# Kernel optimization log

Hardware: AMD Instinct MI355X
Metric: run time of the kernel (lower is better)

Reference implementation:

```python
import jax, jax.numpy as jnp
import numpy as np

B, S, D, H = 2, 2048, 1024, 16
DH = D // H
LN_EPS = 1e-12


def setup_inputs() -> dict:
    key = jax.random.key(0)
    ks = jax.random.split(key, 12)
    sc = 1.0 / np.sqrt(D)
    return {
        "hidden_states": jax.random.normal(ks[0], (B, S, D), jnp.float32),
        "attention_mask": jnp.zeros((B, 1, 1, S), jnp.float32),
        "Wq": jax.random.normal(ks[1], (D, D), jnp.float32) * sc,
        "bq": jnp.zeros((D,), jnp.float32),
        "Wk": jax.random.normal(ks[2], (D, D), jnp.float32) * sc,
        "bk": jnp.zeros((D,), jnp.float32),
        "Wv": jax.random.normal(ks[3], (D, D), jnp.float32) * sc,
        "bv": jnp.zeros((D,), jnp.float32),
        "Wo": jax.random.normal(ks[4], (D, D), jnp.float32) * sc,
        "bo": jnp.zeros((D,), jnp.float32),
        "ln_w": jnp.ones((D,), jnp.float32),
        "ln_b": jnp.zeros((D,), jnp.float32),
    }


def _split_heads(x):
    # [B,S,D] -> [B,H,S,DH]
    return x.reshape(B, S, H, DH).transpose(0, 2, 1, 3)


def reference(hidden_states, attention_mask, Wq, bq, Wk, bk, Wv, bv, Wo, bo, ln_w, ln_b):
    q = _split_heads(hidden_states @ Wq + bq)
    k = _split_heads(hidden_states @ Wk + bk)
    v = _split_heads(hidden_states @ Wv + bv)
    scores = jnp.einsum("bhqd,bhkd->bhqk", q, k) / np.sqrt(DH)
    scores = scores + attention_mask
    probs = jax.nn.softmax(scores, axis=-1)  # dropout prob=0 -> identity
    ctx = jnp.einsum("bhqk,bhkd->bhqd", probs, v)
    ctx = ctx.transpose(0, 2, 1, 3).reshape(B, S, D)
    # output dense + residual + LayerNorm (biased variance, per original)
    h = ctx @ Wo + bo + hidden_states
    u = h.mean(-1, keepdims=True)
    s = ((h - u) ** 2).mean(-1, keepdims=True)
    out = ln_w * ((h - u) / jnp.sqrt(s + LN_EPS)) + ln_b
    return out, probs
```

## Files before the change

### kernel.cpp

```cpp
#include <hip/hip_runtime.h>
#include <stdint.h>


typedef __attribute__((ext_vector_type(8))) short short8;
typedef __attribute__((ext_vector_type(4))) float f32x4;

__device__ __forceinline__ unsigned short f2b(float f) {
  union { float f; unsigned u; } v; v.f = f;
  unsigned u = v.u;
  return (unsigned short)((u + 0x7fffu + ((u >> 16) & 1u)) >> 16);
}

__global__ void k_cast_hs(const float* __restrict__ x, unsigned short* __restrict__ y, int n4) {
  int i = blockIdx.x * blockDim.x + threadIdx.x;
  if (i < n4) {
    float4 v = ((const float4*)x)[i];
    ushort4 o;
    o.x = f2b(v.x); o.y = f2b(v.y); o.z = f2b(v.z); o.w = f2b(v.w);
    ((ushort4*)y)[i] = o;
  }
}

__global__ void k_transpose_cast(const float* __restrict__ Wq, const float* __restrict__ Wk,
                                 const float* __restrict__ Wv, const float* __restrict__ Wo,
                                 unsigned short* __restrict__ Tq, unsigned short* __restrict__ Tk,
                                 unsigned short* __restrict__ Tv, unsigned short* __restrict__ To) {
  __shared__ float tile[32][33];
  const float* W; unsigned short* T;
  switch (blockIdx.z) {
    case 0: W = Wq; T = Tq; break;
    case 1: W = Wk; T = Tk; break;
    case 2: W = Wv; T = Tv; break;
    default: W = Wo; T = To; break;
  }
  int n0 = blockIdx.x * 32, k0 = blockIdx.y * 32;
  int tx = threadIdx.x, ty = threadIdx.y;
#pragma unroll
  for (int j = 0; j < 4; ++j)
    tile[ty + j * 8][tx] = W[(size_t)(k0 + ty + j * 8) * 1024 + n0 + tx];
  __syncthreads();
#pragma unroll
  for (int j = 0; j < 4; ++j)
    T[(size_t)(n0 + ty + j * 8) * 1024 + k0 + tx] = f2b(tile[tx][ty + j * 8]);
}

template <int MODE>
__global__ __launch_bounds__(256) void k_gemm(const unsigned short* __restrict__ A,
                                              const unsigned short* __restrict__ Bt, int Kd,
                                              const float* __restrict__ bias,
                                              const float* __restrict__ resid,
                                              void* __restrict__ outp) {
  __shared__ __align__(16) unsigned short Asm[128 * 32];
  __shared__ __align__(16) unsigned short Bsm[128 * 32];
  const int t = threadIdx.x, w = t >> 6, l = t & 63;
  const int m0 = blockIdx.y * 128, n0 = blockIdx.x * 128;
  const int wr = w >> 1, wc = w & 1;
  const int lr = l & 15, lg = l >> 4;

  f32x4 acc[4][4];
#pragma unroll
  for (int mi = 0; mi < 4; ++mi)
#pragma unroll
    for (int ni = 0; ni < 4; ++ni) acc[mi][ni] = (f32x4){0.f, 0.f, 0.f, 0.f};

  const int kcol = (l & 3) * 8;
  for (int kt = 0; kt < Kd / 32; ++kt) {
    const int k0 = kt * 32;
#pragma unroll
    for (int i = 0; i < 2; ++i) {
      int ra = (i * 4 + w) * 16 + (l >> 2);
      const unsigned short* ga = A + (size_t)(m0 + ra) * Kd + k0 + kcol;
      __builtin_amdgcn_global_load_lds((const __attribute__((address_space(1))) void*)ga,
                                       (__attribute__((address_space(3))) void*)((char*)Asm + (i * 4 + w) * 1024),
                                       16, 0, 0);
      const unsigned short* gb = Bt + (size_t)(n0 + ra) * Kd + k0 + kcol;
      __builtin_amdgcn_global_load_lds((const __attribute__((address_space(1))) void*)gb,
                                       (__attribute__((address_space(3))) void*)((char*)Bsm + (i * 4 + w) * 1024),
                                       16, 0, 0);
    }
    __syncthreads();
    short8 af[4], bfv[4];
#pragma unroll
    for (int mi = 0; mi < 4; ++mi)
      af[mi] = *(const short8*)&Asm[(wr * 64 + mi * 16 + lr) * 32 + lg * 8];
#pragma unroll
    for (int ni = 0; ni < 4; ++ni)
      bfv[ni] = *(const short8*)&Bsm[(wc * 64 + ni * 16 + lr) * 32 + lg * 8];
#pragma unroll
    for (int mi = 0; mi < 4; ++mi)
#pragma unroll
      for (int ni = 0; ni < 4; ++ni)
        acc[mi][ni] = __builtin_amdgcn_mfma_f32_16x16x32_bf16(af[mi], bfv[ni], acc[mi][ni], 0, 0, 0);
    __syncthreads();
  }

#pragma unroll
  for (int mi = 0; mi < 4; ++mi) {
#pragma unroll
    for (int ni = 0; ni < 4; ++ni) {
#pragma unroll
      for (int r = 0; r < 4; ++r) {
        int row = m0 + wr * 64 + mi * 16 + lg * 4 + r;
        int col = n0 + wc * 64 + ni * 16 + lr;
        float v = acc[mi][ni][r];
        if constexpr (MODE == 0) {
          v += bias[col];
          int b = row >> 11, s = row & 2047, h = col >> 6, dh = col & 63;
          ((unsigned short*)outp)[((size_t)((b * 16 + h) * 2048 + s)) * 64 + dh] = f2b(v);
        } else if constexpr (MODE == 1) {
          v += bias[row];
          int h = row >> 6, dh = row & 63, b = col >> 11, s = col & 2047;
          ((unsigned short*)outp)[((size_t)((b * 16 + h) * 64 + dh)) * 2048 + s] = f2b(v);
        } else {
          v += bias[col] + resid[(size_t)row * 1024 + col];
          ((float*)outp)[(size_t)row * 1024 + col] = v;
        }
      }
    }
  }
}

__global__ __launch_bounds__(256) void k_attn(const unsigned short* __restrict__ Q,
                                              const unsigned short* __restrict__ K,
                                              const unsigned short* __restrict__ VT,
                                              const float* __restrict__ mask,
                                              float* __restrict__ probs,
                                              unsigned short* __restrict__ ctx) {
  __shared__ float smax[4][16];
  __shared__ float ssum[4][16];
  __shared__ __align__(16) unsigned short pbuf[4][16][264];
  __shared__ float redbuf[4][16][64];

  const int t = threadIdx.x, w = t >> 6, l = t & 63;
  const int qb = blockIdx.x, h = blockIdx.y, b = blockIdx.z;
  const int q0 = qb * 16;
  const int lr = l & 15, lg = l >> 4;
  const size_t head = ((size_t)(b * 16 + h)) * 2048 * 64;
  const unsigned short* Qh = Q + head + (size_t)q0 * 64;
  const unsigned short* Kh = K + head;
  const unsigned short* VTh = VT + head;

  short8 aq0 = *(const short8*)(Qh + lr * 64 + lg * 8);
  short8 aq1 = *(const short8*)(Qh + lr * 64 + 32 + lg * 8);

  f32x4 sc[32];
  const float scale = 0.125f;
#pragma unroll
  for (int ni = 0; ni < 32; ++ni) {
    int col = w * 512 + ni * 16 + lr;
    short8 bk0 = *(const short8*)(Kh + (size_t)col * 64 + lg * 8);
    short8 bk1 = *(const short8*)(Kh + (size_t)col * 64 + 32 + lg * 8);
    f32x4 c = (f32x4){0.f, 0.f, 0.f, 0.f};
    c = __builtin_amdgcn_mfma_f32_16x16x32_bf16(aq0, bk0, c, 0, 0, 0);
    c = __builtin_amdgcn_mfma_f32_16x16x32_bf16(aq1, bk1, c, 0, 0, 0);
    float mval = mask[b * 2048 + col];
#pragma unroll
    for (int r = 0; r < 4; ++r) sc[ni][r] = c[r] * scale + mval;
  }

  float vmax[4] = {-1e30f, -1e30f, -1e30f, -1e30f};
#pragma unroll
  for (int ni = 0; ni < 32; ++ni)
#pragma unroll
    for (int r = 0; r < 4; ++r) vmax[r] = fmaxf(vmax[r], sc[ni][r]);
#pragma unroll
  for (int off = 8; off >= 1; off >>= 1)
#pragma unroll
    for (int r = 0; r < 4; ++r) vmax[r] = fmaxf(vmax[r], __shfl_xor(vmax[r], off));
  if (lr == 0) {
#pragma unroll
    for (int r = 0; r < 4; ++r) smax[w][lg * 4 + r] = vmax[r];
  }
  __syncthreads();
  float m[4];
#pragma unroll
  for (int r = 0; r < 4; ++r) {
    int row = lg * 4 + r;
    m[r] = fmaxf(fmaxf(smax[0][row], smax[1][row]), fmaxf(smax[2][row], smax[3][row]));
  }
  float vsum[4] = {0.f, 0.f, 0.f, 0.f};
#pragma unroll
  for (int ni = 0; ni < 32; ++ni)
#pragma unroll
    for (int r = 0; r < 4; ++r) {
      float p = __expf(sc[ni][r] - m[r]);
      sc[ni][r] = p;
      vsum[r] += p;
    }
#pragma unroll
  for (int off = 8; off >= 1; off >>= 1)
#pragma unroll
    for (int r = 0; r < 4; ++r) vsum[r] += __shfl_xor(vsum[r], off);
  if (lr == 0) {
#pragma unroll
    for (int r = 0; r < 4; ++r) ssum[w][lg * 4 + r] = vsum[r];
  }
  __syncthreads();
  float rinv[4];
#pragma unroll
  for (int r = 0; r < 4; ++r) {
    int row = lg * 4 + r;
    rinv[r] = 1.f / (ssum[0][row] + ssum[1][row] + ssum[2][row] + ssum[3][row]);
  }

#pragma unroll
  for (int ni = 0; ni < 32; ++ni) {
#pragma unroll
    for (int r = 0; r < 4; ++r) {
      sc[ni][r] *= rinv[r];
      int row = q0 + lg * 4 + r;
      int col = w * 512 + ni * 16 + lr;
      probs[((size_t)((b * 16 + h) * 2048 + row)) * 2048 + col] = sc[ni][r];
    }
  }

  f32x4 cacc[4];
#pragma unroll
  for (int n = 0; n < 4; ++n) cacc[n] = (f32x4){0.f, 0.f, 0.f, 0.f};

#pragma unroll
  for (int chunk = 0; chunk < 2; ++chunk) {
#pragma unroll
    for (int ni2 = 0; ni2 < 16; ++ni2) {
      int ni = chunk * 16 + ni2;
#pragma unroll
      for (int r = 0; r < 4; ++r)
        pbuf[w][lg * 4 + r][ni2 * 16 + lr] = f2b(sc[ni][r]);
    }
    __syncthreads();
#pragma unroll
    for (int kc = 0; kc < 8; ++kc) {
      short8 pa = *(const short8*)&pbuf[w][lr][kc * 32 + lg * 8];
      size_t kg = (size_t)w * 512 + chunk * 256 + kc * 32;
#pragma unroll
      for (int n = 0; n < 4; ++n) {
        short8 bv = *(const short8*)(VTh + (size_t)(n * 16 + lr) * 2048 + kg + lg * 8);
        cacc[n] = __builtin_amdgcn_mfma_f32_16x16x32_bf16(pa, bv, cacc[n], 0, 0, 0);
      }
    }
    __syncthreads();
  }

#pragma unroll
  for (int n = 0; n < 4; ++n)
#pragma unroll
    for (int r = 0; r < 4; ++r)
      redbuf[w][lg * 4 + r][n * 16 + lr] = cacc[n][r];
  __syncthreads();

  {
    int row = t >> 4;
    int c0 = (t & 15) * 4;
    float v0 = redbuf[0][row][c0] + redbuf[1][row][c0] + redbuf[2][row][c0] + redbuf[3][row][c0];
    float v1 = redbuf[0][row][c0 + 1] + redbuf[1][row][c0 + 1] + redbuf[2][row][c0 + 1] + redbuf[3][row][c0 + 1];
    float v2 = redbuf[0][row][c0 + 2] + redbuf[1][row][c0 + 2] + redbuf[2][row][c0 + 2] + redbuf[3][row][c0 + 2];
    float v3 = redbuf[0][row][c0 + 3] + redbuf[1][row][c0 + 3] + redbuf[2][row][c0 + 3] + redbuf[3][row][c0 + 3];
    ushort4 o;
    o.x = f2b(v0); o.y = f2b(v1); o.z = f2b(v2); o.w = f2b(v3);
    *(ushort4*)(ctx + ((size_t)(b * 2048 + q0 + row)) * 1024 + h * 64 + c0) = o;
  }
}

__global__ __launch_bounds__(256) void k_ln(const float* __restrict__ hbuf, const float* __restrict__ g,
                                            const float* __restrict__ be, float* __restrict__ out) {
  __shared__ float psum[4];
  __shared__ float psq[4];
  int tok = blockIdx.x;
  int t = threadIdx.x, w = t >> 6;
  float4 v = ((const float4*)(hbuf + (size_t)tok * 1024))[t];
  float s = v.x + v.y + v.z + v.w;
  float q = v.x * v.x + v.y * v.y + v.z * v.z + v.w * v.w;
#pragma unroll
  for (int off = 32; off >= 1; off >>= 1) {
    s += __shfl_xor(s, off);
    q += __shfl_xor(q, off);
  }
  if ((t & 63) == 0) { psum[w] = s; psq[w] = q; }
  __syncthreads();
  float S = psum[0] + psum[1] + psum[2] + psum[3];
  float Qs = psq[0] + psq[1] + psq[2] + psq[3];
  float u = S * (1.f / 1024.f);
  float var = Qs * (1.f / 1024.f) - u * u;
  float rstd = rsqrtf(var + 1e-12f);
  float4 gv = ((const float4*)g)[t];
  float4 bv = ((const float4*)be)[t];
  float4 o;
  o.x = gv.x * ((v.x - u) * rstd) + bv.x;
  o.y = gv.y * ((v.y - u) * rstd) + bv.y;
  o.z = gv.z * ((v.z - u) * rstd) + bv.z;
  o.w = gv.w * ((v.w - u) * rstd) + bv.w;
  ((float4*)(out + (size_t)tok * 1024))[t] = o;
}

extern "C" void kernel_launch(void* const* d_in, const int* in_sizes, int n_in,
                              void* d_out, int out_size, void* d_ws, size_t ws_size,
                              hipStream_t stream) {
  const float* hs   = (const float*)d_in[0];
  const float* mask = (const float*)d_in[1];
  const float* Wq   = (const float*)d_in[2];
  const float* bq   = (const float*)d_in[3];
  const float* Wk   = (const float*)d_in[4];
  const float* bk   = (const float*)d_in[5];
  const float* Wv   = (const float*)d_in[6];
  const float* bv   = (const float*)d_in[7];
  const float* Wo   = (const float*)d_in[8];
  const float* bo   = (const float*)d_in[9];
  const float* lnw  = (const float*)d_in[10];
  const float* lnb  = (const float*)d_in[11];

  float* out = (float*)d_out;
  float* probs = out + (size_t)4194304;

  char* ws = (char*)d_ws;
  const size_t MB = 1u << 20;
  unsigned short* hsb = (unsigned short*)(ws + 0 * MB);
  unsigned short* TqW = (unsigned short*)(ws + 8 * MB);
  unsigned short* TkW = (unsigned short*)(ws + 10 * MB);
  unsigned short* TvW = (unsigned short*)(ws + 12 * MB);
  unsigned short* ToW = (unsigned short*)(ws + 14 * MB);
  unsigned short* Qb  = (unsigned short*)(ws + 16 * MB);
  unsigned short* Kb  = (unsigned short*)(ws + 24 * MB);
  unsigned short* VTb = (unsigned short*)(ws + 32 * MB);
  unsigned short* ctxb = (unsigned short*)(ws + 40 * MB);
  float* hbuf = (float*)(ws + 48 * MB);

  k_cast_hs<<<4096, 256, 0, stream>>>(hs, hsb, 1048576);
  k_transpose_cast<<<dim3(32, 32, 4), dim3(32, 8), 0, stream>>>(Wq, Wk, Wv, Wo, TqW, TkW, TvW, ToW);

  k_gemm<0><<<dim3(8, 32), 256, 0, stream>>>(hsb, TqW, 1024, bq, nullptr, Qb);
  k_gemm<0><<<dim3(8, 32), 256, 0, stream>>>(hsb, TkW, 1024, bk, nullptr, Kb);
  k_gemm<1><<<dim3(32, 8), 256, 0, stream>>>(TvW, hsb, 1024, bv, nullptr, VTb);

  k_attn<<<dim3(128, 16, 2), 256, 0, stream>>>(Qb, Kb, VTb, mask, probs, ctxb);

  k_gemm<2><<<dim3(8, 32), 256, 0, stream>>>(ctxb, ToW, 1024, bo, hs, hbuf);
  k_ln<<<4096, 256, 0, stream>>>(hbuf, lnw, lnb, out);
}
```

Baseline: 451.2 us.

## Transpose score MFMA to vectorize probs stores and fold scale into Q projection

Swaps the MFMA operand order in the attention score computation so each lane holds four consecutive key columns of one query row. This allows 16-byte vector stores of the probability matrix, vector mask loads, and a simpler per-lane softmax reduction. The 1/sqrt(dh) scale is folded into the Q projection epilogue. The shared buffers for P and the reduction are aliased, a barrier is dropped, and launch bounds request two blocks per CU, which raises occupancy but may cost registers or cause spills. Prescaling Q before the bf16 cast slightly changes rounding.

```diff
diff --git a/kernel.cpp b/kernel.cpp
--- a/kernel.cpp
+++ b/kernel.cpp
@@ -49,7 +49,7 @@
                                               const unsigned short* __restrict__ Bt, int Kd,
                                               const float* __restrict__ bias,
                                               const float* __restrict__ resid,
-                                              void* __restrict__ outp) {
+                                              void* __restrict__ outp, float qscale) {
   __shared__ __align__(16) unsigned short Asm[128 * 32];
   __shared__ __align__(16) unsigned short Bsm[128 * 32];
   const int t = threadIdx.x, w = t >> 6, l = t & 63;
@@ -104,7 +104,7 @@
         int col = n0 + wc * 64 + ni * 16 + lr;
         float v = acc[mi][ni][r];
         if constexpr (MODE == 0) {
-          v += bias[col];
+          v = (v + bias[col]) * qscale;
           int b = row >> 11, s = row & 2047, h = col >> 6, dh = col & 63;
           ((unsigned short*)outp)[((size_t)((b * 16 + h) * 2048 + s)) * 64 + dh] = f2b(v);
         } else if constexpr (MODE == 1) {
@@ -120,16 +120,17 @@
   }
 }
 
-__global__ __launch_bounds__(256) void k_attn(const unsigned short* __restrict__ Q,
-                                              const unsigned short* __restrict__ K,
-                                              const unsigned short* __restrict__ VT,
-                                              const float* __restrict__ mask,
-                                              float* __restrict__ probs,
-                                              unsigned short* __restrict__ ctx) {
+__global__ __launch_bounds__(256, 2) void k_attn(const unsigned short* __restrict__ Q,
+                                                 const unsigned short* __restrict__ K,
+                                                 const unsigned short* __restrict__ VT,
+                                                 const float* __restrict__ mask,
+                                                 float* __restrict__ probs,
+                                                 unsigned short* __restrict__ ctx) {
   __shared__ float smax[4][16];
   __shared__ float ssum[4][16];
-  __shared__ __align__(16) unsigned short pbuf[4][16][264];
-  __shared__ float redbuf[4][16][64];
+  __shared__ __align__(16) char shbuf[33792];
+  unsigned short (*pbuf)[16][264] = (unsigned short(*)[16][264])shbuf;
+  float (*redbuf)[16][64] = (float(*)[16][64])shbuf;
 
   const int t = threadIdx.x, w = t >> 6, l = t & 63;
   const int qb = blockIdx.x, h = blockIdx.y, b = blockIdx.z;
@@ -144,90 +145,68 @@
   short8 aq1 = *(const short8*)(Qh + lr * 64 + 32 + lg * 8);
 
   f32x4 sc[32];
-  const float scale = 0.125f;
 #pragma unroll
   for (int ni = 0; ni < 32; ++ni) {
     int col = w * 512 + ni * 16 + lr;
     short8 bk0 = *(const short8*)(Kh + (size_t)col * 64 + lg * 8);
     short8 bk1 = *(const short8*)(Kh + (size_t)col * 64 + 32 + lg * 8);
     f32x4 c = (f32x4){0.f, 0.f, 0.f, 0.f};
-    c = __builtin_amdgcn_mfma_f32_16x16x32_bf16(aq0, bk0, c, 0, 0, 0);
-    c = __builtin_amdgcn_mfma_f32_16x16x32_bf16(aq1, bk1, c, 0, 0, 0);
-    float mval = mask[b * 2048 + col];
-#pragma unroll
-    for (int r = 0; r < 4; ++r) sc[ni][r] = c[r] * scale + mval;
-  }
-
-  float vmax[4] = {-1e30f, -1e30f, -1e30f, -1e30f};
+    c = __builtin_amdgcn_mfma_f32_16x16x32_bf16(bk0, aq0, c, 0, 0, 0);
+    c = __builtin_amdgcn_mfma_f32_16x16x32_bf16(bk1, aq1, c, 0, 0, 0);
+    f32x4 mv = *(const f32x4*)(mask + b * 2048 + w * 512 + ni * 16 + lg * 4);
+    sc[ni] = c + mv;
+  }
+
+  float vmax = -1e30f;
 #pragma unroll
   for (int ni = 0; ni < 32; ++ni)
 #pragma unroll
-    for (int r = 0; r < 4; ++r) vmax[r] = fmaxf(vmax[r], sc[ni][r]);
-#pragma unroll
-  for (int off = 8; off >= 1; off >>= 1)
-#pragma unroll
-    for (int r = 0; r < 4; ++r) vmax[r] = fmaxf(vmax[r], __shfl_xor(vmax[r], off));
-  if (lr == 0) {
-#pragma unroll
-    for (int r = 0; r < 4; ++r) smax[w][lg * 4 + r] = vmax[r];
-  }
-  __syncthreads();
-  float m[4];
-#pragma unroll
-  for (int r = 0; r < 4; ++r) {
-    int row = lg * 4 + r;
-    m[r] = fmaxf(fmaxf(smax[0][row], smax[1][row]), fmaxf(smax[2][row], smax[3][row]));
-  }
-  float vsum[4] = {0.f, 0.f, 0.f, 0.f};
+    for (int r = 0; r < 4; ++r) vmax = fmaxf(vmax, sc[ni][r]);
+  vmax = fmaxf(vmax, __shfl_xor(vmax, 16));
+  vmax = fmaxf(vmax, __shfl_xor(vmax, 32));
+  if (l < 16) smax[w][l] = vmax;
+  __syncthreads();
+  float m = fmaxf(fmaxf(smax[0][lr], smax[1][lr]), fmaxf(smax[2][lr], smax[3][lr]));
+
+  float vsum = 0.f;
 #pragma unroll
   for (int ni = 0; ni < 32; ++ni)
 #pragma unroll
     for (int r = 0; r < 4; ++r) {
-      float p = __expf(sc[ni][r] - m[r]);
+      float p = __expf(sc[ni][r] - m);
       sc[ni][r] = p;
-      vsum[r] += p;
-    }
-#pragma unroll
-  for (int off = 8; off >= 1; off >>= 1)
-#pragma unroll
-    for (int r = 0; r < 4; ++r) vsum[r] += __shfl_xor(vsum[r], off);
-  if (lr == 0) {
-#pragma unroll
-    for (int r = 0; r < 4; ++r) ssum[w][lg * 4 + r] = vsum[r];
-  }
-  __syncthreads();
-  float rinv[4];
-#pragma unroll
-  for (int r = 0; r < 4; ++r) {
-    int row = lg * 4 + r;
-    rinv[r] = 1.f / (ssum[0][row] + ssum[1][row] + ssum[2][row] + ssum[3][row]);
-  }
-
-#pragma unroll
-  for (int ni = 0; ni < 32; ++ni) {
-#pragma unroll
-    for (int r = 0; r < 4; ++r) {
-      sc[ni][r] *= rinv[r];
-      int row = q0 + lg * 4 + r;
-      int col = w * 512 + ni * 16 + lr;
-      probs[((size_t)((b * 16 + h) * 2048 + row)) * 2048 + col] = sc[ni][r];
-    }
+      vsum += p;
+    }
+  vsum += __shfl_xor(vsum, 16);
+  vsum += __shfl_xor(vsum, 32);
+  if (l < 16) ssum[w][l] = vsum;
+  __syncthreads();
+  float rinv = 1.f / (ssum[0][lr] + ssum[1][lr] + ssum[2][lr] + ssum[3][lr]);
+
+#pragma unroll
+  for (int ni = 0; ni < 32; ++ni) sc[ni] *= rinv;
+
+  {
+    float* prow = probs + ((size_t)((b * 16 + h) * 2048 + q0 + lr)) * 2048 + w * 512 + lg * 4;
+#pragma unroll
+    for (int ni = 0; ni < 32; ++ni)
+      *(f32x4*)(prow + ni * 16) = sc[ni];
   }
 
   f32x4 cacc[4];
 #pragma unroll
   for (int n = 0; n < 4; ++n) cacc[n] = (f32x4){0.f, 0.f, 0.f, 0.f};
 
-#pragma unroll
+#pragma unroll 1
   for (int chunk = 0; chunk < 2; ++chunk) {
 #pragma unroll
     for (int ni2 = 0; ni2 < 16; ++ni2) {
       int ni = chunk * 16 + ni2;
-#pragma unroll
-      for (int r = 0; r < 4; ++r)
-        pbuf[w][lg * 4 + r][ni2 * 16 + lr] = f2b(sc[ni][r]);
-    }
-    __syncthreads();
+      ushort4 pk;
+      pk.x = f2b(sc[ni][0]); pk.y = f2b(sc[ni][1]);
+      pk.z = f2b(sc[ni][2]); pk.w = f2b(sc[ni][3]);
+      *(ushort4*)&pbuf[w][lr][ni2 * 16 + lg * 4] = pk;
+    }
 #pragma unroll
     for (int kc = 0; kc < 8; ++kc) {
       short8 pa = *(const short8*)&pbuf[w][lr][kc * 32 + lg * 8];
@@ -238,8 +217,8 @@
         cacc[n] = __builtin_amdgcn_mfma_f32_16x16x32_bf16(pa, bv, cacc[n], 0, 0, 0);
       }
     }
-    __syncthreads();
-  }
+  }
+  __syncthreads();
 
 #pragma unroll
   for (int n = 0; n < 4; ++n)
@@ -327,12 +306,12 @@
   k_cast_hs<<<4096, 256, 0, stream>>>(hs, hsb, 1048576);
   k_transpose_cast<<<dim3(32, 32, 4), dim3(32, 8), 0, stream>>>(Wq, Wk, Wv, Wo, TqW, TkW, TvW, ToW);
 
-  k_gemm<0><<<dim3(8, 32), 256, 0, stream>>>(hsb, TqW, 1024, bq, nullptr, Qb);
-  k_gemm<0><<<dim3(8, 32), 256, 0, stream>>>(hsb, TkW, 1024, bk, nullptr, Kb);
-  k_gemm<1><<<dim3(32, 8), 256, 0, stream>>>(TvW, hsb, 1024, bv, nullptr, VTb);
+  k_gemm<0><<<dim3(8, 32), 256, 0, stream>>>(hsb, TqW, 1024, bq, nullptr, Qb, 0.125f);
+  k_gemm<0><<<dim3(8, 32), 256, 0, stream>>>(hsb, TkW, 1024, bk, nullptr, Kb, 1.0f);
+  k_gemm<1><<<dim3(32, 8), 256, 0, stream>>>(TvW, hsb, 1024, bv, nullptr, VTb, 1.0f);
 
   k_attn<<<dim3(128, 16, 2), 256, 0, stream>>>(Qb, Kb, VTb, mask, probs, ctxb);
 
-  k_gemm<2><<<dim3(8, 32), 256, 0, stream>>>(ctxb, ToW, 1024, bo, hs, hbuf);
+  k_gemm<2><<<dim3(8, 32), 256, 0, stream>>>(ctxb, ToW, 1024, bo, hs, hbuf, 1.0f);
   k_ln<<<4096, 256, 0, stream>>>(hbuf, lnw, lnb, out);
 }
```

New measurement: 858.8 us. +90.3%, slower.
